# Kernel tuning notes

Hardware: AMD Instinct MI355X
Metric: run time of the kernel (lower is better)

## Reference

```python
import jax, jax.numpy as jnp
import numpy as np

B, P, G, H, W = 4, 24, 24, 512, 512
IOU_THRESH = 0.5
SMOOTH = 1.0
LOG_CLAMP = -100.0  # torch F.binary_cross_entropy clamps log terms at -100


def _pairwise_iou(pb, gb):
    # pb: [B,P,4], gb: [B,G,4]; boxes are (y1,x1,y2,x2), normalized
    a = pb[:, :, None, :]  # [B,P,1,4]
    b = gb[:, None, :, :]  # [B,1,G,4]
    area_a = (a[..., 2] - a[..., 0]) * (a[..., 3] - a[..., 1])
    area_b = (b[..., 2] - b[..., 0]) * (b[..., 3] - b[..., 1])
    int_h = jnp.maximum(jnp.minimum(a[..., 2], b[..., 2]) - jnp.maximum(a[..., 0], b[..., 0]), 0.0)
    int_w = jnp.maximum(jnp.minimum(a[..., 3], b[..., 3]) - jnp.maximum(a[..., 1], b[..., 1]), 0.0)
    inter = int_h * int_w
    union = area_a + area_b - inter
    return jnp.where(union == 0.0, 0.0, inter / jnp.where(union == 0.0, 1.0, union))  # [B,P,G]


def _seg_loss(pred_masks, pred_boxes, gt_boxes, gt_masks, pred_valid, gt_valid):
    # IoU matching (argmax over gt, keep if max IoU >= 0.5)
    iou = _pairwise_iou(pred_boxes, gt_boxes)                      # [B,P,G]
    iou = jnp.where(gt_valid[:, None, :], iou, -1.0)
    max_iou = jnp.max(iou, axis=-1)                                # [B,P]
    gt_idx = jnp.argmax(iou, axis=-1)                              # [B,P]
    keep = (max_iou >= IOU_THRESH) & pred_valid                    # [B,P]

    # integer crop coords, matching np.round (half-to-even) + clamping of the source
    y1 = jnp.maximum(0, jnp.round(pred_boxes[..., 0] * H).astype(jnp.int32))
    x1 = jnp.maximum(0, jnp.round(pred_boxes[..., 1] * W).astype(jnp.int32))
    y2 = jnp.minimum(jnp.round(pred_boxes[..., 2] * H).astype(jnp.int32), H - 1)
    x2 = jnp.minimum(jnp.round(pred_boxes[..., 3] * W).astype(jnp.int32), W - 1)

    rows = jnp.arange(H)[None, None, :, None]                      # [1,1,H,1]
    cols = jnp.arange(W)[None, None, None, :]                      # [1,1,1,W]
    region = ((rows >= y1[..., None, None]) & (rows <= y2[..., None, None]) &
              (cols >= x1[..., None, None]) & (cols <= x2[..., None, None]))
    rf = region.astype(pred_masks.dtype)                           # [B,P,H,W]

    # gather matched gt masks: [B,P,H,W]
    t = jnp.take_along_axis(gt_masks, gt_idx[:, :, None, None], axis=1)
    p = pred_masks

    # BCE over the crop region (mean over crop pixels)
    logp = jnp.clip(jnp.log(p), LOG_CLAMP)
    log1mp = jnp.clip(jnp.log1p(-p), LOG_CLAMP)
    bce_px = -(t * logp + (1.0 - t) * log1mp) * rf
    cnt = jnp.sum(rf, axis=(2, 3))                                 # [B,P]
    bce = jnp.sum(bce_px, axis=(2, 3)) / jnp.maximum(cnt, 1.0)

    # Dice over the crop region
    pr = p * rf
    tr = t * rf
    inter = jnp.sum(pr * tr, axis=(2, 3))
    dice = 1.0 - (2.0 * inter + SMOOTH) / (jnp.sum(pr, axis=(2, 3)) + jnp.sum(tr, axis=(2, 3)) + SMOOTH)

    loss_obj = bce + dice                                          # [B,P]
    n_obj = jnp.sum(keep.astype(jnp.float32))
    total = jnp.sum(jnp.where(keep, loss_obj, 0.0))
    return total / jnp.maximum(n_obj, 1.0)


def setup_inputs() -> dict:
    key = jax.random.key(0)
    k0, k1, k2, k3, k4, k5, k6 = jax.random.split(key, 7)
    # valid gt boxes: size in [0.1, 0.5], fully inside the unit square
    sz = jax.random.uniform(k0, (B, G, 2), minval=0.1, maxval=0.5)
    tl = jax.random.uniform(k1, (B, G, 2)) * (1.0 - sz)
    gt_boxes = jnp.concatenate([tl, tl + sz], axis=-1).astype(jnp.float32)  # (y1,x1,y2,x2)
    # predictions = jittered gt boxes so IoU>=0.5 matches occur
    raw = gt_boxes + 0.02 * jax.random.normal(k2, (B, P, 4))
    pred_boxes = jnp.clip(jnp.concatenate([jnp.minimum(raw[..., :2], raw[..., 2:]),
                                           jnp.maximum(raw[..., :2], raw[..., 2:])], axis=-1), 0.0, 1.0)
    pred_boxes = pred_boxes.astype(jnp.float32)
    pred_masks = jax.random.uniform(k3, (B, P, H, W), minval=1e-4, maxval=1.0 - 1e-4, dtype=jnp.float32)
    gt_masks = (jax.random.uniform(k4, (B, G, H, W)) > 0.5).astype(jnp.float32)
    pred_valid = jax.random.uniform(k5, (B, P)) > 0.2
    gt_valid = jax.random.uniform(k6, (B, G)) > 0.2
    return {"pred_masks": pred_masks, "pred_boxes": pred_boxes, "gt_boxes": gt_boxes,
            "gt_masks": gt_masks, "pred_valid": pred_valid, "gt_valid": gt_valid}


def reference(pred_masks, pred_boxes, gt_boxes, gt_masks, pred_valid, gt_valid):
    return _seg_loss(pred_masks, pred_boxes, gt_boxes, gt_masks, pred_valid, gt_valid)
```

## Files before the change

### kernel.cpp

```cpp
#include <hip/hip_runtime.h>
#include <math.h>

#define Bn 4
#define Pn 24
#define Gn 24
#define Hd 512
#define Wd 512
#define NOBJ (Bn * Pn)
#define SPLIT 8
#define IOU_THRESH 0.5f

#define AUX_OFF (NOBJ * SPLIT * 4)

__device__ __forceinline__ void match_obj(const float* __restrict__ pred_boxes,
                                          const float* __restrict__ gt_boxes,
                                          const int* __restrict__ pred_valid,
                                          const int* __restrict__ gt_valid,
                                          int obj, int& keep, int& gidx,
                                          int& y1, int& x1, int& y2, int& x2) {
    int b = obj / Pn;
    const float* pb = pred_boxes + (size_t)obj * 4;
    float a0 = pb[0], a1 = pb[1], a2 = pb[2], a3 = pb[3];
    float area_a = (a2 - a0) * (a3 - a1);
    float best = -1.0f;
    gidx = 0;
    #pragma unroll
    for (int g = 0; g < Gn; ++g) {
        const float* gb = gt_boxes + ((size_t)b * Gn + g) * 4;
        float b0 = gb[0], b1 = gb[1], b2 = gb[2], b3 = gb[3];
        float area_b = (b2 - b0) * (b3 - b1);
        float ih = fmaxf(fminf(a2, b2) - fmaxf(a0, b0), 0.0f);
        float iw = fmaxf(fminf(a3, b3) - fmaxf(a1, b1), 0.0f);
        float inter = ih * iw;
        float uni = area_a + area_b - inter;
        float iou = (uni == 0.0f) ? 0.0f : inter / uni;
        if (gt_valid[b * Gn + g] == 0) iou = -1.0f;
        if (iou > best) { best = iou; gidx = g; }
    }
    keep = (best >= IOU_THRESH) && (pred_valid[obj] != 0);
    y1 = max(0, (int)rintf(a0 * (float)Hd));
    x1 = max(0, (int)rintf(a1 * (float)Wd));
    y2 = min((int)rintf(a2 * (float)Hd), Hd - 1);
    x2 = min((int)rintf(a3 * (float)Wd), Wd - 1);
}

__global__ __launch_bounds__(256) void region_kernel(
    const float* __restrict__ pred_masks, const float* __restrict__ gt_masks,
    const float* __restrict__ pred_boxes, const float* __restrict__ gt_boxes,
    const int* __restrict__ pred_valid, const int* __restrict__ gt_valid,
    float* __restrict__ acc, float* __restrict__ aux) {
    int obj = blockIdx.x;
    int part = blockIdx.y;

    int keep, gidx, y1, x1, y2, x2;
    match_obj(pred_boxes, gt_boxes, pred_valid, gt_valid, obj, keep, gidx, y1, x1, y2, x2);

    float v0 = 0.0f, v1 = 0.0f, v2 = 0.0f, v3 = 0.0f;
    if (keep && y2 >= y1 && x2 >= x1) {
        int Wr = x2 - x1 + 1;
        int Hr = y2 - y1 + 1;
        int x1a = x1 & ~3;
        int W4 = (x2 >> 2) - (x1 >> 2) + 1;
        int N4 = Hr * W4;
        int idx = part * 256 + (int)threadIdx.x;
        if (idx < N4) {
            const float* pm = pred_masks + (size_t)obj * Hd * Wd + x1a;
            const float* gm = gt_masks + ((size_t)(obj / Pn) * Gn + gidx) * Hd * Wd + x1a;
            const int step = SPLIT * 256;
            int r = idx / W4;
            int c = idx - r * W4;
            int dr = step / W4;
            int dc = step - dr * W4;
            int rel0 = x1a - x1;

            int off = (y1 + r) * Wd + (c << 2);
            float4 p4 = *reinterpret_cast<const float4*>(pm + off);
            float4 q4 = *reinterpret_cast<const float4*>(gm + off);
            int rel = rel0 + (c << 2);
            while (true) {
                idx += step;
                bool more = idx < N4;
                float4 p4n, q4n;
                int reln = 0;
                if (more) {
                    c += dc; r += dr;
                    if (c >= W4) { c -= W4; ++r; }
                    int offn = (y1 + r) * Wd + (c << 2);
                    p4n = *reinterpret_cast<const float4*>(pm + offn);
                    q4n = *reinterpret_cast<const float4*>(gm + offn);
                    reln = rel0 + (c << 2);
                }
                bool m0 = (unsigned)(rel + 0) < (unsigned)Wr;
                bool m1 = (unsigned)(rel + 1) < (unsigned)Wr;
                bool m2 = (unsigned)(rel + 2) < (unsigned)Wr;
                bool m3 = (unsigned)(rel + 3) < (unsigned)Wr;
                float p0 = m0 ? p4.x : 0.0f, q0 = m0 ? q4.x : 0.0f;
                float p1 = m1 ? p4.y : 0.0f, q1 = m1 ? q4.y : 0.0f;
                float p2 = m2 ? p4.z : 0.0f, q2 = m2 ? q4.z : 0.0f;
                float p3 = m3 ? p4.w : 0.0f, q3 = m3 ? q4.w : 0.0f;
                float a0 = (q0 > 0.5f) ? p0 : 1.0f - p0;
                float a1 = (q1 > 0.5f) ? p1 : 1.0f - p1;
                float a2 = (q2 > 0.5f) ? p2 : 1.0f - p2;
                float a3 = (q3 > 0.5f) ? p3 : 1.0f - p3;
                v0 -= __logf((a0 * a1) * (a2 * a3));
                v1 = fmaf(p0, q0, fmaf(p1, q1, fmaf(p2, q2, fmaf(p3, q3, v1))));
                v2 += (p0 + p1) + (p2 + p3);
                v3 += (q0 + q1) + (q2 + q3);
                if (!more) break;
                p4 = p4n; q4 = q4n; rel = reln;
            }
        }
    }

    for (int o = 32; o > 0; o >>= 1) {
        v0 += __shfl_down(v0, o, 64);
        v1 += __shfl_down(v1, o, 64);
        v2 += __shfl_down(v2, o, 64);
        v3 += __shfl_down(v3, o, 64);
    }
    __shared__ float red[4][4];
    int lane = threadIdx.x & 63, w = threadIdx.x >> 6;
    if (lane == 0) { red[w][0] = v0; red[w][1] = v1; red[w][2] = v2; red[w][3] = v3; }
    __syncthreads();
    if (threadIdx.x < 4) {
        float sfin = red[0][threadIdx.x] + red[1][threadIdx.x] +
                     red[2][threadIdx.x] + red[3][threadIdx.x];
        acc[((size_t)obj * SPLIT + part) * 4 + threadIdx.x] = sfin;
    } else if (part == 0 && threadIdx.x == 4) {
        float cnt = (y2 >= y1 && x2 >= x1)
                      ? (float)((y2 - y1 + 1) * (x2 - x1 + 1)) : 0.0f;
        aux[obj * 2 + 0] = keep ? 1.0f : 0.0f;
        aux[obj * 2 + 1] = cnt;
    }
}

__global__ __launch_bounds__(128) void finalize_kernel(
    const float* __restrict__ acc, const float* __restrict__ aux,
    float* __restrict__ out) {
    int i = threadIdx.x;
    float loss = 0.0f, nk = 0.0f;
    if (i < NOBJ) {
        float keepf = aux[i * 2 + 0];
        float cnt = aux[i * 2 + 1];
        if (keepf > 0.5f) {
            nk = 1.0f;
            const float4* a = reinterpret_cast<const float4*>(acc) + (size_t)i * SPLIT;
            float s0 = 0.0f, s1 = 0.0f, s2 = 0.0f, s3 = 0.0f;
            #pragma unroll
            for (int p = 0; p < SPLIT; ++p) {
                float4 v = a[p];
                s0 += v.x; s1 += v.y; s2 += v.z; s3 += v.w;
            }
            float bce = s0 / fmaxf(cnt, 1.0f);
            float dice = 1.0f - (2.0f * s1 + 1.0f) / (s2 + s3 + 1.0f);
            loss = bce + dice;
        }
    }
    float v0 = loss, v1 = nk;
    for (int o = 32; o > 0; o >>= 1) {
        v0 += __shfl_down(v0, o, 64);
        v1 += __shfl_down(v1, o, 64);
    }
    __shared__ float red[2][2];
    if ((threadIdx.x & 63) == 0) { red[threadIdx.x >> 6][0] = v0; red[threadIdx.x >> 6][1] = v1; }
    __syncthreads();
    if (threadIdx.x == 0) {
        float total = red[0][0] + red[1][0];
        float nobj = red[0][1] + red[1][1];
        out[0] = total / fmaxf(nobj, 1.0f);
    }
}

extern "C" void kernel_launch(void* const* d_in, const int* in_sizes, int n_in,
                              void* d_out, int out_size, void* d_ws, size_t ws_size,
                              hipStream_t stream) {
    const float* pred_masks = (const float*)d_in[0];
    const float* pred_boxes = (const float*)d_in[1];
    const float* gt_boxes   = (const float*)d_in[2];
    const float* gt_masks   = (const float*)d_in[3];
    const int*   pred_valid = (const int*)d_in[4];
    const int*   gt_valid   = (const int*)d_in[5];
    float* out = (float*)d_out;
    float* acc = (float*)d_ws;
    float* aux = acc + AUX_OFF;

    region_kernel<<<dim3(NOBJ, SPLIT), 256, 0, stream>>>(
        pred_masks, gt_masks, pred_boxes, gt_boxes, pred_valid, gt_valid, acc, aux);
    finalize_kernel<<<1, 128, 0, stream>>>(acc, aux, out);
}
```

Measured before the change: 15.85 us.

## Fuse finalize into region kernel via last-block atomic ticket

Replaces the separate finalize launch with a last-block-done pattern: each block stores its partial sums, takes an atomic ticket, and the final block recomputes matching per object and reduces the loss. This removes one kernel launch and the gap between launches, but adds a hipMemsetAsync for the counter and relies on relaxed atomics plus an explicit s_waitcnt for ordering. The memset is itself a queued operation, so the saving depends on it costing less than the dropped kernel launch.

```diff
diff --git a/kernel.cpp b/kernel.cpp
--- a/kernel.cpp
+++ b/kernel.cpp
@@ -8,9 +8,10 @@
 #define Wd 512
 #define NOBJ (Bn * Pn)
 #define SPLIT 8
+#define TOTAL (NOBJ * SPLIT)
 #define IOU_THRESH 0.5f
 
-#define AUX_OFF (NOBJ * SPLIT * 4)
+#define ACC_BYTE_OFF 64
 
 __device__ __forceinline__ void match_obj(const float* __restrict__ pred_boxes,
                                           const float* __restrict__ gt_boxes,
@@ -44,11 +45,12 @@
     x2 = min((int)rintf(a3 * (float)Wd), Wd - 1);
 }
 
-__global__ __launch_bounds__(256) void region_kernel(
+__global__ __launch_bounds__(256) void fused_kernel(
     const float* __restrict__ pred_masks, const float* __restrict__ gt_masks,
     const float* __restrict__ pred_boxes, const float* __restrict__ gt_boxes,
     const int* __restrict__ pred_valid, const int* __restrict__ gt_valid,
-    float* __restrict__ acc, float* __restrict__ aux) {
+    float* __restrict__ acc, unsigned int* __restrict__ counter,
+    float* __restrict__ out) {
     int obj = blockIdx.x;
     int part = blockIdx.y;
 
@@ -122,52 +124,62 @@
     int lane = threadIdx.x & 63, w = threadIdx.x >> 6;
     if (lane == 0) { red[w][0] = v0; red[w][1] = v1; red[w][2] = v2; red[w][3] = v3; }
     __syncthreads();
+
+    int bid = obj * SPLIT + part;
     if (threadIdx.x < 4) {
-        float sfin = red[0][threadIdx.x] + red[1][threadIdx.x] +
-                     red[2][threadIdx.x] + red[3][threadIdx.x];
-        acc[((size_t)obj * SPLIT + part) * 4 + threadIdx.x] = sfin;
-    } else if (part == 0 && threadIdx.x == 4) {
-        float cnt = (y2 >= y1 && x2 >= x1)
-                      ? (float)((y2 - y1 + 1) * (x2 - x1 + 1)) : 0.0f;
-        aux[obj * 2 + 0] = keep ? 1.0f : 0.0f;
-        aux[obj * 2 + 1] = cnt;
-    }
-}
-
-__global__ __launch_bounds__(128) void finalize_kernel(
-    const float* __restrict__ acc, const float* __restrict__ aux,
-    float* __restrict__ out) {
-    int i = threadIdx.x;
-    float loss = 0.0f, nk = 0.0f;
-    if (i < NOBJ) {
-        float keepf = aux[i * 2 + 0];
-        float cnt = aux[i * 2 + 1];
-        if (keepf > 0.5f) {
-            nk = 1.0f;
-            const float4* a = reinterpret_cast<const float4*>(acc) + (size_t)i * SPLIT;
-            float s0 = 0.0f, s1 = 0.0f, s2 = 0.0f, s3 = 0.0f;
-            #pragma unroll
-            for (int p = 0; p < SPLIT; ++p) {
-                float4 v = a[p];
-                s0 += v.x; s1 += v.y; s2 += v.z; s3 += v.w;
+        float s = red[0][threadIdx.x] + red[1][threadIdx.x] +
+                  red[2][threadIdx.x] + red[3][threadIdx.x];
+        __hip_atomic_store(&acc[(size_t)bid * 4 + threadIdx.x], s,
+                           __ATOMIC_RELAXED, __HIP_MEMORY_SCOPE_AGENT);
+    }
+    __shared__ unsigned int tkt;
+    if (threadIdx.x == 0) {
+        asm volatile("s_waitcnt vmcnt(0)" ::: "memory");
+        tkt = __hip_atomic_fetch_add(counter, 1u, __ATOMIC_RELAXED,
+                                     __HIP_MEMORY_SCOPE_AGENT);
+    }
+    __syncthreads();
+
+    if (tkt == TOTAL - 1) {
+        int i = (int)threadIdx.x;
+        float loss = 0.0f, nk = 0.0f;
+        if (i < NOBJ) {
+            int k2, g2, yy1, xx1, yy2, xx2;
+            match_obj(pred_boxes, gt_boxes, pred_valid, gt_valid, i,
+                      k2, g2, yy1, xx1, yy2, xx2);
+            if (k2) {
+                nk = 1.0f;
+                float s0 = 0.0f, s1 = 0.0f, s2 = 0.0f, s3 = 0.0f;
+                const float* sl = acc + (size_t)i * SPLIT * 4;
+                #pragma unroll
+                for (int p = 0; p < SPLIT; ++p) {
+                    s0 += __hip_atomic_load(&sl[p * 4 + 0], __ATOMIC_RELAXED, __HIP_MEMORY_SCOPE_AGENT);
+                    s1 += __hip_atomic_load(&sl[p * 4 + 1], __ATOMIC_RELAXED, __HIP_MEMORY_SCOPE_AGENT);
+                    s2 += __hip_atomic_load(&sl[p * 4 + 2], __ATOMIC_RELAXED, __HIP_MEMORY_SCOPE_AGENT);
+                    s3 += __hip_atomic_load(&sl[p * 4 + 3], __ATOMIC_RELAXED, __HIP_MEMORY_SCOPE_AGENT);
+                }
+                float cnt = (yy2 >= yy1 && xx2 >= xx1)
+                              ? (float)((yy2 - yy1 + 1) * (xx2 - xx1 + 1)) : 0.0f;
+                float bce = s0 / fmaxf(cnt, 1.0f);
+                float dice = 1.0f - (2.0f * s1 + 1.0f) / (s2 + s3 + 1.0f);
+                loss = bce + dice;
             }
-            float bce = s0 / fmaxf(cnt, 1.0f);
-            float dice = 1.0f - (2.0f * s1 + 1.0f) / (s2 + s3 + 1.0f);
-            loss = bce + dice;
-        }
-    }
-    float v0 = loss, v1 = nk;
-    for (int o = 32; o > 0; o >>= 1) {
-        v0 += __shfl_down(v0, o, 64);
-        v1 += __shfl_down(v1, o, 64);
-    }
-    __shared__ float red[2][2];
-    if ((threadIdx.x & 63) == 0) { red[threadIdx.x >> 6][0] = v0; red[threadIdx.x >> 6][1] = v1; }
-    __syncthreads();
-    if (threadIdx.x == 0) {
-        float total = red[0][0] + red[1][0];
-        float nobj = red[0][1] + red[1][1];
-        out[0] = total / fmaxf(nobj, 1.0f);
+        }
+        for (int o = 32; o > 0; o >>= 1) {
+            loss += __shfl_down(loss, o, 64);
+            nk += __shfl_down(nk, o, 64);
+        }
+        __shared__ float red2[2][4];
+        if ((threadIdx.x & 63) == 0) {
+            red2[0][threadIdx.x >> 6] = loss;
+            red2[1][threadIdx.x >> 6] = nk;
+        }
+        __syncthreads();
+        if (threadIdx.x == 0) {
+            float total = red2[0][0] + red2[0][1] + red2[0][2] + red2[0][3];
+            float n = red2[1][0] + red2[1][1] + red2[1][2] + red2[1][3];
+            out[0] = total / fmaxf(n, 1.0f);
+        }
     }
 }
 
@@ -181,10 +193,12 @@
     const int*   pred_valid = (const int*)d_in[4];
     const int*   gt_valid   = (const int*)d_in[5];
     float* out = (float*)d_out;
-    float* acc = (float*)d_ws;
-    float* aux = acc + AUX_OFF;
-
-    region_kernel<<<dim3(NOBJ, SPLIT), 256, 0, stream>>>(
-        pred_masks, gt_masks, pred_boxes, gt_boxes, pred_valid, gt_valid, acc, aux);
-    finalize_kernel<<<1, 128, 0, stream>>>(acc, aux, out);
+
+    unsigned int* counter = (unsigned int*)d_ws;
+    float* acc = (float*)((char*)d_ws + ACC_BYTE_OFF);
+
+    hipMemsetAsync(counter, 0, sizeof(unsigned int), stream);
+    fused_kernel<<<dim3(NOBJ, SPLIT), 256, 0, stream>>>(
+        pred_masks, gt_masks, pred_boxes, gt_boxes, pred_valid, gt_valid,
+        acc, counter, out);
 }
```

Result: slower. 27.70 us (+74.8%).
